# Kernel tuning notes

Hardware: AMD Instinct MI355X
Metric: run time of the kernel (lower is better)

Reference implementation:

```python
import jax, jax.numpy as jnp
import numpy as np

SEQ, EMB, OUT = 8192, 1024, 128

def setup_inputs() -> dict:
    key = jax.random.key(0)
    k1, k2, k3, k4 = jax.random.split(key, 4)
    return {
        "x": jax.random.normal(k1, (SEQ, EMB), dtype=jnp.float32),
        "wquery": jax.random.normal(k2, (EMB, OUT), dtype=jnp.float32) * (2.0 / EMB) ** 0.5,
        "wkey": jax.random.normal(k3, (EMB, OUT), dtype=jnp.float32) * (2.0 / EMB) ** 0.5,
        "wvalue": jax.random.normal(k4, (EMB, OUT), dtype=jnp.float32) * (2.0 / EMB) ** 0.5,
    }

def reference(x, wquery, wkey, wvalue):
    # Single-head attention, mask=True branch (mask tensor is zeros -> no masking).
    q = x @ wquery   # [S, D]
    k = x @ wkey     # [S, D]
    v = x @ wvalue   # [S, D]
    scale = jnp.sqrt(jnp.asarray(q.shape[-1], dtype=q.dtype))
    a = (q @ k.T) / scale              # [S, S]
    p = jax.nn.softmax(a, axis=1)      # softmax over keys (dim=1 in torch)
    return p @ v                       # [S, D]
```

## Files before the change

### kernel.cpp

```cpp
#include <hip/hip_runtime.h>
#include <cstdint>
#include <cstddef>

#define SEQ 8192
#define EMB 1024
#define DH  128

typedef __bf16 bf16x8 __attribute__((ext_vector_type(8)));
typedef __bf16 bf16x2 __attribute__((ext_vector_type(2)));
typedef float  f32x4  __attribute__((ext_vector_type(4)));
typedef float  f32x16 __attribute__((ext_vector_type(16)));
typedef uint32_t u32x4 __attribute__((ext_vector_type(4)));
typedef unsigned short u16x8 __attribute__((ext_vector_type(8)));

static constexpr float QSCALE = (float)(1.4426950408889634 / 11.313708498984760);

__device__ __forceinline__ unsigned short f2bf(float f) {
  uint32_t u = __builtin_bit_cast(uint32_t, f);
  u += 0x7FFFu + ((u >> 16) & 1u);
  return (unsigned short)(u >> 16);
}

#define GLD_LDS16(gsrc, ldst) \
  __builtin_amdgcn_global_load_lds((__attribute__((address_space(1))) void*)(gsrc), \
                                   (__attribute__((address_space(3))) void*)(ldst), 16, 0, 0)

__global__ __launch_bounds__(256) void convert_kernel(
    const float* __restrict__ x,
    const float* __restrict__ wq, const float* __restrict__ wk, const float* __restrict__ wv,
    unsigned short* __restrict__ xb, unsigned short* __restrict__ wt)
{
  const int bid = blockIdx.x;
  const int t = threadIdx.x;
  if (bid < 2048) {
    size_t e = (size_t)bid * 4096 + (size_t)t * 16;
#pragma unroll
    for (int i = 0; i < 2; ++i) {
      float4 a = *reinterpret_cast<const float4*>(x + e + i * 8);
      float4 b = *reinterpret_cast<const float4*>(x + e + i * 8 + 4);
      u16x8 o = { f2bf(a.x), f2bf(a.y), f2bf(a.z), f2bf(a.w),
                  f2bf(b.x), f2bf(b.y), f2bf(b.z), f2bf(b.w) };
      *reinterpret_cast<u16x8*>(xb + e + i * 8) = o;
    }
  } else {
    const int which = (bid - 2048) >> 2;
    const int k = ((bid - 2048) & 3) * 256 + t;
    const float* w = (which == 0) ? wq : ((which == 1) ? wk : wv);
    const float scl = (which == 0) ? QSCALE : 1.0f;
#pragma unroll
    for (int n = 0; n < 128; n += 4) {
      float4 v = *reinterpret_cast<const float4*>(w + (size_t)k * DH + n);
      wt[((size_t)which * DH + n + 0) * EMB + k] = f2bf(v.x * scl);
      wt[((size_t)which * DH + n + 1) * EMB + k] = f2bf(v.y * scl);
      wt[((size_t)which * DH + n + 2) * EMB + k] = f2bf(v.z * scl);
      wt[((size_t)which * DH + n + 3) * EMB + k] = f2bf(v.w * scl);
    }
  }
}

__global__ __launch_bounds__(256) void qkv_gemm(
    const unsigned short* __restrict__ xb, const unsigned short* __restrict__ wt,
    unsigned short* __restrict__ qs, unsigned short* __restrict__ ks,
    unsigned short* __restrict__ vt)
{
  __shared__ char LDS[49152];
  char* A0 = LDS;
  char* B0 = LDS + 16384;
  unsigned short* T = (unsigned short*)LDS;

  const int t    = threadIdx.x;
  const int lane = t & 63;
  const int wid  = t >> 6;
  const int wr   = wid >> 1, wc = wid & 1;
  const int l31  = lane & 31;
  const int hi   = lane >> 5;
  const int row0 = blockIdx.x * 64;
  const int which = blockIdx.y;

  const char* xc  = (const char*)xb;
  const char* wtc = (const char*)(wt + (size_t)which * DH * EMB);

  f32x16 acc[2] = {};

  auto STAGE = [&](int buf, int k0) {
#pragma unroll
    for (int i = 0; i < 2; ++i) {
      int bidx = i * 4096 + t * 16;
      int row = bidx >> 7, off = bidx & 127;
      const char* src = xc + (size_t)(row0 + row) * (EMB * 2) + k0 * 2 + (off ^ ((row & 7) << 4));
      GLD_LDS16(src, A0 + buf * 8192 + i * 4096 + wid * 1024);
    }
#pragma unroll
    for (int i = 0; i < 4; ++i) {
      int bidx = i * 4096 + t * 16;
      int n = bidx >> 7, off = bidx & 127;
      const char* src = wtc + (size_t)n * (EMB * 2) + k0 * 2 + (off ^ ((n & 7) << 4));
      GLD_LDS16(src, B0 + buf * 16384 + i * 4096 + wid * 1024);
    }
  };

  STAGE(0, 0);
  int cur = 0;
  for (int it = 0; it < EMB / 64; ++it) {
    if (it + 1 < EMB / 64) {
      STAGE(cur ^ 1, (it + 1) * 64);
      asm volatile("s_waitcnt vmcnt(6)" ::: "memory");
    } else {
      asm volatile("s_waitcnt vmcnt(0)" ::: "memory");
    }
    __builtin_amdgcn_s_barrier();
    asm volatile("" ::: "memory");

    const char* Ab = A0 + cur * 8192;
    const char* Bb = B0 + cur * 16384;
    const int ar   = wr * 32 + l31;
    const int aswz = (l31 & 7) << 4;

    __builtin_amdgcn_s_setprio(1);
#pragma unroll
    for (int kk = 0; kk < 4; ++kk) {
      bf16x8 af = *reinterpret_cast<const bf16x8*>(Ab + ar * 128 + ((kk * 32 + hi * 16) ^ aswz));
#pragma unroll
      for (int nt = 0; nt < 2; ++nt) {
        const int n = wc * 64 + nt * 32 + l31;
        bf16x8 bf = *reinterpret_cast<const bf16x8*>(Bb + n * 128 + ((kk * 32 + hi * 16) ^ ((n & 7) << 4)));
        acc[nt] = __builtin_amdgcn_mfma_f32_32x32x16_bf16(af, bf, acc[nt], 0, 0, 0);
      }
    }
    __builtin_amdgcn_s_setprio(0);

    asm volatile("" ::: "memory");
    __builtin_amdgcn_s_barrier();
    asm volatile("" ::: "memory");
    cur ^= 1;
  }

  if (which < 2) {
    unsigned short* dst = (which == 0) ? qs : ks;
#pragma unroll
    for (int nt = 0; nt < 2; ++nt)
#pragma unroll
      for (int r = 0; r < 16; ++r) {
        int row = row0 + wr * 32 + (r & 3) + 8 * (r >> 2) + 4 * hi;
        dst[(size_t)row * DH + wc * 64 + nt * 32 + l31] = f2bf(acc[nt][r]);
      }
  } else {
    __syncthreads();
#pragma unroll
    for (int nt = 0; nt < 2; ++nt)
#pragma unroll
      for (int r = 0; r < 16; ++r) {
        int d  = wc * 64 + nt * 32 + l31;
        int rl = wr * 32 + (r & 3) + 8 * (r >> 2) + 4 * hi;
        T[d * 72 + rl] = f2bf(acc[nt][r]);
      }
    __syncthreads();
    const int d = t >> 1, half = t & 1;
#pragma unroll
    for (int i = 0; i < 4; ++i) {
      uint4 v = *reinterpret_cast<const uint4*>(&T[d * 72 + half * 32 + i * 8]);
      *reinterpret_cast<uint4*>(vt + (size_t)d * SEQ + row0 + half * 32 + i * 8) = v;
    }
  }
}

template <int NS>
__global__ __launch_bounds__(512, 2) void attn_kernel(
    const unsigned short* __restrict__ qs, const unsigned short* __restrict__ ks,
    const unsigned short* __restrict__ vt,
    float* __restrict__ Op, float* __restrict__ ml)
{
  __shared__ unsigned short Ks[2][64 * 128];
  __shared__ unsigned short Vt[2][128 * 64];

  const int t    = threadIdx.x;
  const int lane = t & 63;
  const int wid  = t >> 6;
  const int l31  = lane & 31;
  const int hi   = lane >> 5;
  const int swz  = (lane & 7) << 4;
  const int q0   = blockIdx.x * 256 + wid * 32;
  const int sp   = blockIdx.y;

  bf16x8 qf[8];
  {
    const unsigned short* qp = qs + (size_t)(q0 + l31) * DH + hi * 8;
#pragma unroll
    for (int ds = 0; ds < 8; ++ds)
      qf[ds] = *reinterpret_cast<const bf16x8*>(qp + ds * 16);
  }

  float m = -__builtin_inff();
  float l = 0.f;
  f32x16 O[4] = {};

  const char* ksc = (const char*)ks;
  const char* vtc = (const char*)vt;
  char* ksl = (char*)&Ks[0][0];
  char* vtl = (char*)&Vt[0][0];

  constexpr int CHUNK = SEQ / NS;
  constexpr int NT = CHUNK / 64;
  const int kv_base = sp * CHUNK;

  auto STAGE = [&](int buf, int it) {
    const int kv0 = kv_base + it * 64;
#pragma unroll
    for (int rr = 0; rr < 2; ++rr) {
      int bidx = rr * 512 + t;
      int key = bidx >> 4, blk = bidx & 15;
      const char* src = ksc + (size_t)(kv0 + key) * 256 + ((blk * 16) ^ ((key & 7) << 4));
      GLD_LDS16(src, ksl + buf * 16384 + rr * 8192 + wid * 1024);
    }
#pragma unroll
    for (int rr = 0; rr < 2; ++rr) {
      int bidx = rr * 512 + t;
      int d = bidx >> 3, kb = bidx & 7;
      const char* src = vtc + (size_t)d * (SEQ * 2) + (size_t)kv0 * 2 + ((kb * 16) ^ ((d & 7) << 4));
      GLD_LDS16(src, vtl + buf * 16384 + rr * 8192 + wid * 1024);
    }
  };

  auto build2 = [&](const f32x16& P, bf16x8* fr) {
    uint32_t c[8];
#pragma unroll
    for (int i = 0; i < 8; ++i) {
      bf16x2 b2; b2[0] = (__bf16)P[2 * i]; b2[1] = (__bf16)P[2 * i + 1];
      c[i] = __builtin_bit_cast(uint32_t, b2);
    }
    uint32_t r0 = __shfl_xor(c[0], 32, 64), r1 = __shfl_xor(c[1], 32, 64);
    uint32_t r2 = __shfl_xor(c[2], 32, 64), r3 = __shfl_xor(c[3], 32, 64);
    u32x4 w0;
    w0[0] = hi ? r2 : c[0];
    w0[1] = hi ? r3 : c[1];
    w0[2] = hi ? c[2] : r0;
    w0[3] = hi ? c[3] : r1;
    uint32_t r4 = __shfl_xor(c[4], 32, 64), r5 = __shfl_xor(c[5], 32, 64);
    uint32_t r6 = __shfl_xor(c[6], 32, 64), r7 = __shfl_xor(c[7], 32, 64);
    u32x4 w1;
    w1[0] = hi ? r6 : c[4];
    w1[1] = hi ? r7 : c[5];
    w1[2] = hi ? c[6] : r4;
    w1[3] = hi ? c[7] : r5;
    fr[0] = __builtin_bit_cast(bf16x8, w0);
    fr[1] = __builtin_bit_cast(bf16x8, w1);
  };

  STAGE(0, 0);

  int cur = 0;
  for (int it = 0; it < NT; ++it) {
    if (it + 1 < NT) {
      STAGE(cur ^ 1, it + 1);
      asm volatile("s_waitcnt vmcnt(4)" ::: "memory");
    } else {
      asm volatile("s_waitcnt vmcnt(0)" ::: "memory");
    }
    __builtin_amdgcn_s_barrier();
    asm volatile("" ::: "memory");

    const char* kbase = ksl + cur * 16384;
    const char* vbase = vtl + cur * 16384;

    f32x16 S0 = {}, S1 = {};
    __builtin_amdgcn_s_setprio(1);
#pragma unroll
    for (int ds = 0; ds < 8; ++ds) {
      bf16x8 ka = *reinterpret_cast<const bf16x8*>(kbase + l31 * 256 + ((ds * 32 + hi * 16) ^ swz));
      S0 = __builtin_amdgcn_mfma_f32_32x32x16_bf16(ka, qf[ds], S0, 0, 0, 0);
    }
#pragma unroll
    for (int ds = 0; ds < 8; ++ds) {
      bf16x8 ka = *reinterpret_cast<const bf16x8*>(kbase + 8192 + l31 * 256 + ((ds * 32 + hi * 16) ^ swz));
      S1 = __builtin_amdgcn_mfma_f32_32x32x16_bf16(ka, qf[ds], S1, 0, 0, 0);
    }
    __builtin_amdgcn_s_setprio(0);

    float pm;
    {
      float a = S0[0];
#pragma unroll
      for (int r = 1; r < 16; ++r) a = fmaxf(a, S0[r]);
#pragma unroll
      for (int r = 0; r < 16; ++r) a = fmaxf(a, S1[r]);
      pm = fmaxf(a, __shfl_xor(a, 32, 64));
    }
    if (__any(pm > m + 11.0f)) {
      float mn = fmaxf(m, pm);
      float corr = __builtin_amdgcn_exp2f(m - mn);
      m = mn;
      l *= corr;
#pragma unroll
      for (int r = 0; r < 16; ++r) {
        float cr = __shfl(corr, (r & 3) + 8 * (r >> 2) + 4 * hi, 64);
#pragma unroll
        for (int nt = 0; nt < 4; ++nt) O[nt][r] *= cr;
      }
    }
    float rsum = 0.f;
#pragma unroll
    for (int r = 0; r < 16; ++r) { S0[r] = __builtin_amdgcn_exp2f(S0[r] - m); rsum += S0[r]; }
#pragma unroll
    for (int r = 0; r < 16; ++r) { S1[r] = __builtin_amdgcn_exp2f(S1[r] - m); rsum += S1[r]; }
    l += rsum + __shfl_xor(rsum, 32, 64);

    bf16x8 pa[4];
    build2(S0, &pa[0]);
    build2(S1, &pa[2]);

    __builtin_amdgcn_s_setprio(1);
#pragma unroll
    for (int ks4 = 0; ks4 < 4; ++ks4) {
#pragma unroll
      for (int nt = 0; nt < 4; ++nt) {
        const int d = nt * 32 + l31;
        bf16x8 vb = *reinterpret_cast<const bf16x8*>(vbase + d * 128 + ((ks4 * 32 + hi * 16) ^ swz));
        O[nt] = __builtin_amdgcn_mfma_f32_32x32x16_bf16(pa[ks4], vb, O[nt], 0, 0, 0);
      }
    }
    __builtin_amdgcn_s_setprio(0);

    asm volatile("" ::: "memory");
    __builtin_amdgcn_s_barrier();
    asm volatile("" ::: "memory");
    cur ^= 1;
  }

  float* Obase = Op + ((size_t)sp * SEQ + q0) * DH;
#pragma unroll
  for (int nt = 0; nt < 4; ++nt)
#pragma unroll
    for (int r = 0; r < 16; ++r) {
      int row = (r & 3) + 8 * (r >> 2) + 4 * hi;
      Obase[(size_t)row * DH + nt * 32 + l31] = O[nt][r];
    }
  if (lane < 32) {
    ml[(size_t)sp * (2 * SEQ) + q0 + lane]       = m;
    ml[(size_t)sp * (2 * SEQ) + SEQ + q0 + lane] = l;
  }
}

template <int NS>
__global__ __launch_bounds__(256) void combine_kernel(
    const float* __restrict__ Op, const float* __restrict__ ml, float* __restrict__ out)
{
  const int idx = blockIdx.x * 256 + threadIdx.x;
  const int s = idx >> 5;
  const int c = (idx & 31) * 4;
  float mv[NS], lv[NS];
  float M = -__builtin_inff();
#pragma unroll
  for (int i = 0; i < NS; ++i) {
    mv[i] = ml[(size_t)i * (2 * SEQ) + s];
    lv[i] = ml[(size_t)i * (2 * SEQ) + SEQ + s];
    M = fmaxf(M, mv[i]);
  }
  float den = 0.f;
  f32x4 num = {};
#pragma unroll
  for (int i = 0; i < NS; ++i) {
    float w = __builtin_amdgcn_exp2f(mv[i] - M);
    den += w * lv[i];
    f32x4 o = *reinterpret_cast<const f32x4*>(&Op[((size_t)i * SEQ + s) * DH + c]);
#pragma unroll
    for (int j = 0; j < 4; ++j) num[j] += w * o[j];
  }
  const float inv = 1.f / den;
  f32x4 res;
#pragma unroll
  for (int j = 0; j < 4; ++j) res[j] = num[j] * inv;
  *reinterpret_cast<f32x4*>(&out[(size_t)s * DH + c]) = res;
}

extern "C" void kernel_launch(void* const* d_in, const int* in_sizes, int n_in,
                              void* d_out, int out_size, void* d_ws, size_t ws_size,
                              hipStream_t stream) {
  const float* x  = (const float*)d_in[0];
  const float* wq = (const float*)d_in[1];
  const float* wk = (const float*)d_in[2];
  const float* wv = (const float*)d_in[3];
  float* out = (float*)d_out;

  char* ws = (char*)d_ws;
  const size_t MB = 1024 * 1024;
  unsigned short* qs = (unsigned short*)(ws);
  unsigned short* ks = (unsigned short*)(ws + 2 * MB);
  unsigned short* vt = (unsigned short*)(ws + 4 * MB);
  unsigned short* wt = (unsigned short*)(ws + 6 * MB);
  float* ml          = (float*)(ws + 6 * MB);
  unsigned short* xb = (unsigned short*)(ws + 6 * MB + 768 * 1024);
  float* Op          = (float*)xb;

  convert_kernel<<<2048 + 12, 256, 0, stream>>>(x, wq, wk, wv, xb, wt);
  qkv_gemm<<<dim3(SEQ / 64, 3), 256, 0, stream>>>(xb, wt, qs, ks, vt);

  const size_t base = 6 * MB + 768 * 1024;
  if (ws_size >= base + 32ull * MB + 8ull * 2 * SEQ * 4) {
    attn_kernel<8><<<dim3(SEQ / 256, 8), 512, 0, stream>>>(qs, ks, vt, Op, ml);
    combine_kernel<8><<<SEQ * DH / 4 / 256, 256, 0, stream>>>(Op, ml, out);
  } else {
    attn_kernel<4><<<dim3(SEQ / 256, 4), 512, 0, stream>>>(qs, ks, vt, Op, ml);
    combine_kernel<4><<<SEQ * DH / 4 / 256, 256, 0, stream>>>(Op, ml, out);
  }
}
```

Measured before the change: 88.16 us.

## Raise split-K to 16, store normalized bf16 partials, tree-reduce softmax stats

```diff
diff --git a/kernel.cpp b/kernel.cpp
--- a/kernel.cpp
+++ b/kernel.cpp
@@ -19,6 +19,9 @@
   uint32_t u = __builtin_bit_cast(uint32_t, f);
   u += 0x7FFFu + ((u >> 16) & 1u);
   return (unsigned short)(u >> 16);
+}
+__device__ __forceinline__ float bf2f(unsigned short u) {
+  return __builtin_bit_cast(float, (uint32_t)u << 16);
 }
 
 #define GLD_LDS16(gsrc, ldst) \
@@ -165,10 +168,10 @@
 }
 
 template <int NS>
-__global__ __launch_bounds__(512, 2) void attn_kernel(
+__global__ __launch_bounds__(512, 4) void attn_kernel(
     const unsigned short* __restrict__ qs, const unsigned short* __restrict__ ks,
     const unsigned short* __restrict__ vt,
-    float* __restrict__ Op, float* __restrict__ ml)
+    unsigned short* __restrict__ Obf, float* __restrict__ ml)
 {
   __shared__ unsigned short Ks[2][64 * 128];
   __shared__ unsigned short Vt[2][128 * 64];
@@ -276,15 +279,15 @@
     }
     __builtin_amdgcn_s_setprio(0);
 
-    float pm;
-    {
-      float a = S0[0];
-#pragma unroll
-      for (int r = 1; r < 16; ++r) a = fmaxf(a, S0[r]);
-#pragma unroll
-      for (int r = 0; r < 16; ++r) a = fmaxf(a, S1[r]);
-      pm = fmaxf(a, __shfl_xor(a, 32, 64));
-    }
+    float mx[16];
+#pragma unroll
+    for (int r = 0; r < 16; ++r) mx[r] = fmaxf(S0[r], S1[r]);
+#pragma unroll
+    for (int st = 8; st >= 1; st >>= 1)
+#pragma unroll
+      for (int r = 0; r < st; ++r) mx[r] = fmaxf(mx[r], mx[r + st]);
+    const float pm = fmaxf(mx[0], __shfl_xor(mx[0], 32, 64));
+
     if (__any(pm > m + 11.0f)) {
       float mn = fmaxf(m, pm);
       float corr = __builtin_amdgcn_exp2f(m - mn);
@@ -297,12 +300,18 @@
         for (int nt = 0; nt < 4; ++nt) O[nt][r] *= cr;
       }
     }
-    float rsum = 0.f;
-#pragma unroll
-    for (int r = 0; r < 16; ++r) { S0[r] = __builtin_amdgcn_exp2f(S0[r] - m); rsum += S0[r]; }
-#pragma unroll
-    for (int r = 0; r < 16; ++r) { S1[r] = __builtin_amdgcn_exp2f(S1[r] - m); rsum += S1[r]; }
-    l += rsum + __shfl_xor(rsum, 32, 64);
+    float sm[16];
+#pragma unroll
+    for (int r = 0; r < 16; ++r) {
+      S0[r] = __builtin_amdgcn_exp2f(S0[r] - m);
+      S1[r] = __builtin_amdgcn_exp2f(S1[r] - m);
+      sm[r] = S0[r] + S1[r];
+    }
+#pragma unroll
+    for (int st = 8; st >= 1; st >>= 1)
+#pragma unroll
+      for (int r = 0; r < st; ++r) sm[r] += sm[r + st];
+    l += sm[0] + __shfl_xor(sm[0], 32, 64);
 
     bf16x8 pa[4];
     build2(S0, &pa[0]);
@@ -326,14 +335,16 @@
     cur ^= 1;
   }
 
-  float* Obase = Op + ((size_t)sp * SEQ + q0) * DH;
-#pragma unroll
-  for (int nt = 0; nt < 4; ++nt)
-#pragma unroll
-    for (int r = 0; r < 16; ++r) {
-      int row = (r & 3) + 8 * (r >> 2) + 4 * hi;
-      Obase[(size_t)row * DH + nt * 32 + l31] = O[nt][r];
-    }
+  const float linv = 1.0f / l;
+  unsigned short* Obase = Obf + ((size_t)sp * SEQ + q0) * DH;
+#pragma unroll
+  for (int r = 0; r < 16; ++r) {
+    const int row = (r & 3) + 8 * (r >> 2) + 4 * hi;
+    const float li = __shfl(linv, row, 64);
+#pragma unroll
+    for (int nt = 0; nt < 4; ++nt)
+      Obase[(size_t)row * DH + nt * 32 + l31] = f2bf(O[nt][r] * li);
+  }
   if (lane < 32) {
     ml[(size_t)sp * (2 * SEQ) + q0 + lane]       = m;
     ml[(size_t)sp * (2 * SEQ) + SEQ + q0 + lane] = l;
@@ -342,11 +353,11 @@
 
 template <int NS>
 __global__ __launch_bounds__(256) void combine_kernel(
-    const float* __restrict__ Op, const float* __restrict__ ml, float* __restrict__ out)
+    const unsigned short* __restrict__ Obf, const float* __restrict__ ml, float* __restrict__ out)
 {
   const int idx = blockIdx.x * 256 + threadIdx.x;
-  const int s = idx >> 5;
-  const int c = (idx & 31) * 4;
+  const int s = idx >> 4;
+  const int c = (idx & 15) * 8;
   float mv[NS], lv[NS];
   float M = -__builtin_inff();
 #pragma unroll
@@ -356,20 +367,21 @@
     M = fmaxf(M, mv[i]);
   }
   float den = 0.f;
-  f32x4 num = {};
+  float num[8] = {};
 #pragma unroll
   for (int i = 0; i < NS; ++i) {
-    float w = __builtin_amdgcn_exp2f(mv[i] - M);
-    den += w * lv[i];
-    f32x4 o = *reinterpret_cast<const f32x4*>(&Op[((size_t)i * SEQ + s) * DH + c]);
-#pragma unroll
-    for (int j = 0; j < 4; ++j) num[j] += w * o[j];
+    float g = __builtin_amdgcn_exp2f(mv[i] - M) * lv[i];
+    den += g;
+    u16x8 o = *reinterpret_cast<const u16x8*>(&Obf[((size_t)i * SEQ + s) * DH + c]);
+#pragma unroll
+    for (int j = 0; j < 8; ++j) num[j] += g * bf2f(o[j]);
   }
   const float inv = 1.f / den;
-  f32x4 res;
-#pragma unroll
-  for (int j = 0; j < 4; ++j) res[j] = num[j] * inv;
-  *reinterpret_cast<f32x4*>(&out[(size_t)s * DH + c]) = res;
+  f32x4 r0, r1;
+#pragma unroll
+  for (int j = 0; j < 4; ++j) { r0[j] = num[j] * inv; r1[j] = num[j + 4] * inv; }
+  *reinterpret_cast<f32x4*>(&out[(size_t)s * DH + c])     = r0;
+  *reinterpret_cast<f32x4*>(&out[(size_t)s * DH + c + 4]) = r1;
 }
 
 extern "C" void kernel_launch(void* const* d_in, const int* in_sizes, int n_in,
@@ -387,19 +399,25 @@
   unsigned short* ks = (unsigned short*)(ws + 2 * MB);
   unsigned short* vt = (unsigned short*)(ws + 4 * MB);
   unsigned short* wt = (unsigned short*)(ws + 6 * MB);
-  float* ml          = (float*)(ws + 6 * MB);
   unsigned short* xb = (unsigned short*)(ws + 6 * MB + 768 * 1024);
-  float* Op          = (float*)xb;
 
   convert_kernel<<<2048 + 12, 256, 0, stream>>>(x, wq, wk, wv, xb, wt);
   qkv_gemm<<<dim3(SEQ / 64, 3), 256, 0, stream>>>(xb, wt, qs, ks, vt);
 
-  const size_t base = 6 * MB + 768 * 1024;
-  if (ws_size >= base + 32ull * MB + 8ull * 2 * SEQ * 4) {
-    attn_kernel<8><<<dim3(SEQ / 256, 8), 512, 0, stream>>>(qs, ks, vt, Op, ml);
-    combine_kernel<8><<<SEQ * DH / 4 / 256, 256, 0, stream>>>(Op, ml, out);
+  unsigned short* Obf = (unsigned short*)(ws + 6 * MB);
+  const size_t need16 = 6 * MB + 16ull * SEQ * DH * 2 + 16ull * 2 * SEQ * 4;
+  const size_t need8  = 6 * MB +  8ull * SEQ * DH * 2 +  8ull * 2 * SEQ * 4;
+  if (ws_size >= need16) {
+    float* ml = (float*)(ws + 6 * MB + 16ull * SEQ * DH * 2);
+    attn_kernel<16><<<dim3(SEQ / 256, 16), 512, 0, stream>>>(qs, ks, vt, Obf, ml);
+    combine_kernel<16><<<SEQ * DH / 8 / 256, 256, 0, stream>>>(Obf, ml, out);
+  } else if (ws_size >= need8) {
+    float* ml = (float*)(ws + 6 * MB + 8ull * SEQ * DH * 2);
+    attn_kernel<8><<<dim3(SEQ / 256, 8), 512, 0, stream>>>(qs, ks, vt, Obf, ml);
+    combine_kernel<8><<<SEQ * DH / 8 / 256, 256, 0, stream>>>(Obf, ml, out);
   } else {
-    attn_kernel<4><<<dim3(SEQ / 256, 4), 512, 0, stream>>>(qs, ks, vt, Op, ml);
-    combine_kernel<4><<<SEQ * DH / 4 / 256, 256, 0, stream>>>(Op, ml, out);
-  }
-}
+    float* ml = (float*)(ws + 6 * MB + 4ull * SEQ * DH * 2);
+    attn_kernel<4><<<dim3(SEQ / 256, 4), 512, 0, stream>>>(qs, ks, vt, Obf, ml);
+    combine_kernel<4><<<SEQ * DH / 8 / 256, 256, 0, stream>>>(Obf, ml, out);
+  }
+}
```

New measurement: 150.8 us. 71.1% more time.
